# Kernel optimization log

Hardware: AMD Instinct MI355X
Metric: run time of the kernel (lower is better)

Reference implementation:

```python
import jax, jax.numpy as jnp
import numpy as np

B, V, F = 128, 256, 64      # batch, vertices, features-per-vertex
NS, NLR, K, NOUT = 4, 64, 40, 128
F_EFF = 2 * F               # cat_means doubles feature dim


def setup_inputs() -> dict:
    key = jax.random.key(0)
    k0, k1, k2 = jax.random.split(key, 3)
    x = jax.random.normal(k0, (B, V, F), dtype=jnp.float32)
    # f_slr: single Linear(F_EFF, NS+NLR) + ReLU (f_slr_depth=1)
    W_slr = jax.random.normal(k1, (F_EFF, NS + NLR), dtype=jnp.float32) / np.sqrt(F_EFF).astype(np.float32)
    b_slr = jnp.zeros((NS + NLR,), dtype=jnp.float32)
    # f_out: single Linear(F_EFF + 2*NLR, NOUT) + ReLU (f_out_depth=1, 2 agg methods)
    fin = F_EFF + 2 * NLR
    W_out = jax.random.normal(k2, (fin, NOUT), dtype=jnp.float32) / np.sqrt(fin).astype(np.float32)
    b_out = jnp.zeros((NOUT,), dtype=jnp.float32)
    return {"x": x, "W_slr": W_slr, "b_slr": b_slr, "W_out": W_out, "b_out": b_out}


def reference(x, W_slr, b_slr, W_out, b_out):
    # cat_means: append per-event feature means (broadcast over vertices)
    x = jnp.concatenate([x, jnp.broadcast_to(x.mean(axis=1, keepdims=True), x.shape)], axis=-1)  # (B,V,2F)
    slr = jax.nn.relu(x @ W_slr + b_slr)                    # (B,V,NS+NLR)
    s, lr = slr[..., :NS], slr[..., NS:]
    # pairwise squared distances in latent space (potential only needs d^2, so
    # we skip the sqrt: exp(-10*d^2) == exp(-10*d2), and kNN order is identical)
    diff = s[:, :, None, :] - s[:, None, :, :]              # (B,V,V,NS)
    d2 = jnp.sum(diff * diff, axis=-1)                      # (B,V,V)
    _, idx = jax.lax.top_k(-d2, K)                          # (B,V,K) k smallest (incl. self)
    d2k = jnp.take_along_axis(d2, idx, axis=2)              # (B,V,K)
    lr_nb = jax.vmap(lambda l, i: l[i])(lr, idx)            # (B,V,K,NLR)
    v = jnp.exp(-10.0 * d2k)                                # potential exp(-10 d^2)
    ft = lr_nb * v[..., None]                               # (B,V,K,NLR)
    fp = jnp.concatenate([x, ft.mean(axis=2), ft.max(axis=2)], axis=-1)  # (B,V,2F+2NLR)
    return jax.nn.relu(fp @ W_out + b_out)                  # (B,V,NOUT)
```

## Files before the change

### kernel.cpp

```cpp
#include <hip/hip_runtime.h>

constexpr int Bn = 128, Vn = 256, Fn = 64;
constexpr int NSLR = 68, NSn = 4, NLRn = 64;
constexpr int Kn = 40, NOUTn = 128;
constexpr int ROWS = Bn * Vn;

typedef __attribute__((ext_vector_type(8))) short short8;
typedef __attribute__((ext_vector_type(4))) float f32x4;

__device__ __forceinline__ int mbcnt64(unsigned long long m) {
  return __builtin_amdgcn_mbcnt_hi((unsigned)(m >> 32),
         __builtin_amdgcn_mbcnt_lo((unsigned)(m & 0xFFFFFFFFull), 0));
}

__device__ __forceinline__ unsigned short rneb(float v) {
  unsigned u = __float_as_uint(v);
  unsigned r = u + 0x7FFFu + ((u >> 16) & 1u);
  return (unsigned short)(r >> 16);
}
__device__ __forceinline__ float bf2f(unsigned short h) {
  return __uint_as_float(((unsigned)h) << 16);
}

__global__ __launch_bounds__(256) void kprep_w(const float* __restrict__ W_slr,
                                               const float* __restrict__ W_out,
                                               short* __restrict__ wt1h, short* __restrict__ wt1l,
                                               short* __restrict__ wt2h, short* __restrict__ wt2l) {
  int id = blockIdx.x * 256 + threadIdx.x;
  if (id < 16384) {
    int col = id >> 7, k = id & 127;
    float val = (col < NSLR) ? W_slr[k * NSLR + col] : 0.f;
    unsigned short h = rneb(val);
    unsigned short lo = rneb(val - bf2f(h));
    wt1h[id] = (short)h; wt1l[id] = (short)lo;
  } else {
    int id2 = id - 16384;
    int col = id2 >> 8, k = id2 & 255;
    float val = W_out[k * NOUTn + col];
    unsigned short h = rneb(val);
    unsigned short lo = rneb(val - bf2f(h));
    wt2h[id2] = (short)h; wt2l[id2] = (short)lo;
  }
}

__global__ __launch_bounds__(256) void kprep_x(const float* __restrict__ x,
                                               short* __restrict__ xhi, short* __restrict__ xlo,
                                               short* __restrict__ xmhi, short* __restrict__ xmlo) {
  const int b = blockIdx.x, t = threadIdx.x, f = t & 63, vg = t >> 6;
  const float* xb = x + (size_t)b * 16384;
  float sum = 0.f;
  for (int i = 0; i < 64; ++i) {
    int v = vg * 64 + i;
    float val = xb[v * 64 + f];
    sum += val;
    unsigned short h = rneb(val);
    unsigned short lo = rneb(val - bf2f(h));
    size_t o = (size_t)b * 16384 + v * 64 + f;
    xhi[o] = (short)h; xlo[o] = (short)lo;
  }
  __shared__ float ps[4][64];
  ps[vg][f] = sum;
  __syncthreads();
  if (t < 64) {
    float m = ((ps[0][f] + ps[1][f]) + (ps[2][f] + ps[3][f])) * (1.f / 256.f);
    unsigned short h = rneb(m);
    unsigned short lo = rneb(m - bf2f(h));
    xmhi[b * 64 + f] = (short)h; xmlo[b * 64 + f] = (short)lo;
  }
}

template <int NCH, bool IS_OUT>
__global__ __launch_bounds__(512) void kgemm_mfma(
    const short* __restrict__ xhi, const short* __restrict__ xlo,
    const short* __restrict__ xmhi, const short* __restrict__ xmlo,
    const short* __restrict__ fmh, const short* __restrict__ fml,
    const short* __restrict__ fxh, const short* __restrict__ fxl,
    const short* __restrict__ wth, const short* __restrict__ wtl,
    const float* __restrict__ bias,
    float* __restrict__ s_ws, float* __restrict__ lr_ws,
    float* __restrict__ outp) {
  constexpr int KTOT = NCH * 64;
  __shared__ __align__(16) short Ah[8192], Al[8192], Bh[8192], Bl[8192];
  const int t = threadIdx.x;
  const int l = t & 63;
  const int w = t >> 6;
  const int wr = w >> 2, wc = w & 3;
  const int rowBase = blockIdx.x * 128;
  const int b = rowBase >> 8;

  f32x4 acc[4][2];
#pragma unroll
  for (int mf = 0; mf < 4; ++mf)
#pragma unroll
    for (int nf = 0; nf < 2; ++nf) acc[mf][nf] = (f32x4)(0.f);

  const int lr8 = l >> 3;
  const int ul = (l & 7) ^ lr8;

#pragma unroll
  for (int kc = 0; kc < NCH; ++kc) {
    __syncthreads();
#pragma unroll
    for (int rep = 0; rep < 2; ++rep) {
      const int s = w + rep * 8;
      const int arow = s * 8 + lr8;
      const short *gah, *gal;
      if (kc == 0)      { size_t o = (size_t)(rowBase + arow) * 64 + ul * 8; gah = xhi + o;  gal = xlo + o; }
      else if (kc == 1) { size_t o = (size_t)b * 64 + ul * 8;                gah = xmhi + o; gal = xmlo + o; }
      else if (kc == 2) { size_t o = (size_t)(rowBase + arow) * 64 + ul * 8; gah = fmh + o;  gal = fml + o; }
      else              { size_t o = (size_t)(rowBase + arow) * 64 + ul * 8; gah = fxh + o;  gal = fxl + o; }
      __builtin_amdgcn_global_load_lds((const __attribute__((address_space(1))) void*)gah,
                                       (__attribute__((address_space(3))) void*)&Ah[s * 512], 16, 0, 0);
      __builtin_amdgcn_global_load_lds((const __attribute__((address_space(1))) void*)gal,
                                       (__attribute__((address_space(3))) void*)&Al[s * 512], 16, 0, 0);
      const short* gbh = wth + (size_t)arow * KTOT + kc * 64 + ul * 8;
      const short* gbl = wtl + (size_t)arow * KTOT + kc * 64 + ul * 8;
      __builtin_amdgcn_global_load_lds((const __attribute__((address_space(1))) void*)gbh,
                                       (__attribute__((address_space(3))) void*)&Bh[s * 512], 16, 0, 0);
      __builtin_amdgcn_global_load_lds((const __attribute__((address_space(1))) void*)gbl,
                                       (__attribute__((address_space(3))) void*)&Bl[s * 512], 16, 0, 0);
    }
    __syncthreads();
#pragma unroll
    for (int ks = 0; ks < 2; ++ks) {
      const int pu = (ks * 4 + (l >> 4)) ^ (l & 7);
      short8 ah[4], al[4], bh[2], bl[2];
#pragma unroll
      for (int mf = 0; mf < 4; ++mf) {
        int row = wr * 64 + mf * 16 + (l & 15);
        ah[mf] = *(const short8*)&Ah[row * 64 + pu * 8];
        al[mf] = *(const short8*)&Al[row * 64 + pu * 8];
      }
#pragma unroll
      for (int nf = 0; nf < 2; ++nf) {
        int col = wc * 32 + nf * 16 + (l & 15);
        bh[nf] = *(const short8*)&Bh[col * 64 + pu * 8];
        bl[nf] = *(const short8*)&Bl[col * 64 + pu * 8];
      }
#pragma unroll
      for (int mf = 0; mf < 4; ++mf)
#pragma unroll
        for (int nf = 0; nf < 2; ++nf) {
          acc[mf][nf] = __builtin_amdgcn_mfma_f32_16x16x32_bf16(ah[mf], bh[nf], acc[mf][nf], 0, 0, 0);
          acc[mf][nf] = __builtin_amdgcn_mfma_f32_16x16x32_bf16(ah[mf], bl[nf], acc[mf][nf], 0, 0, 0);
          acc[mf][nf] = __builtin_amdgcn_mfma_f32_16x16x32_bf16(al[mf], bh[nf], acc[mf][nf], 0, 0, 0);
        }
    }
  }
#pragma unroll
  for (int mf = 0; mf < 4; ++mf)
#pragma unroll
    for (int nf = 0; nf < 2; ++nf) {
      const int col = wc * 32 + nf * 16 + (l & 15);
      if (IS_OUT) {
        const float bia = bias[col];
#pragma unroll
        for (int r = 0; r < 4; ++r) {
          int row = rowBase + wr * 64 + mf * 16 + (l >> 4) * 4 + r;
          float vv = acc[mf][nf][r] + bia;
          outp[(size_t)row * NOUTn + col] = vv > 0.f ? vv : 0.f;
        }
      } else {
        if (col < NSLR) {
          const float bia = bias[col];
#pragma unroll
          for (int r = 0; r < 4; ++r) {
            int row = rowBase + wr * 64 + mf * 16 + (l >> 4) * 4 + r;
            float vv = acc[mf][nf][r] + bia;
            vv = vv > 0.f ? vv : 0.f;
            if (col < NSn) s_ws[b * 1024 + col * 256 + (row & 255)] = vv;
            else           lr_ws[(size_t)row * NLRn + (col - NSn)] = vv;
          }
        }
      }
    }
}

__global__ __launch_bounds__(256) void kselect(const float* __restrict__ s_ws,
                                               const float* __restrict__ lr_ws,
                                               short* __restrict__ fmh, short* __restrict__ fml,
                                               short* __restrict__ fxh, short* __restrict__ fxl) {
  __shared__ float sT[4][256];
  __shared__ unsigned int lst[4][Kn];
  const int id = blockIdx.x;
  const int xcd = id & 7;
  const int rrx = id >> 3;
  const int b = xcd + 8 * (rrx & 15);
  const int seg = rrx >> 4;
  const int t = threadIdx.x;
  const int lane = t & 63;
  const int w = t >> 6;

  {
    const float* sb = s_ws + b * 1024;
    sT[0][t] = sb[t]; sT[1][t] = sb[256 + t];
    sT[2][t] = sb[512 + t]; sT[3][t] = sb[768 + t];
  }
  __syncthreads();

  const float C = -14.4269504088896340736f;
  const float* lrbase = lr_ws + (size_t)b * (256 * NLRn) + lane;

  for (int it = 0; it < 4; ++it) {
    const int i = seg * 16 + w * 4 + it;
    const float si0 = sT[0][i], si1 = sT[1][i];
    const float si2 = sT[2][i], si3 = sT[3][i];
    unsigned int kb[4];
    float vv[4];
#pragma unroll
    for (int q = 0; q < 4; ++q) {
      int j = q * 64 + lane;
      float d0 = sT[0][j] - si0;
      float d1 = sT[1][j] - si1;
      float d2_ = sT[2][j] - si2;
      float d3 = sT[3][j] - si3;
      float dd = ((d0 * d0 + d1 * d1) + d2_ * d2_) + d3 * d3;
      kb[q] = __float_as_uint(dd);
      vv[q] = exp2f(C * dd);
    }
    unsigned int T = 0;
    for (int bit = 30; bit >= 0; --bit) {
      unsigned int cand = T | (1u << bit);
      int cnt = __popcll(__ballot(kb[0] < cand)) + __popcll(__ballot(kb[1] < cand)) +
                __popcll(__ballot(kb[2] < cand)) + __popcll(__ballot(kb[3] < cand));
      if (cnt < Kn) T = cand;
    }
    int nlt = __popcll(__ballot(kb[0] < T)) + __popcll(__ballot(kb[1] < T)) +
              __popcll(__ballot(kb[2] < T)) + __popcll(__ballot(kb[3] < T));
    int rem = Kn - nlt;
    int base = 0, ecum = 0;
#pragma unroll
    for (int q = 0; q < 4; ++q) {
      bool lt = kb[q] < T;
      bool eq = kb[q] == T;
      unsigned long long meq = __ballot(eq);
      int eqrank = ecum + mbcnt64(meq);
      bool sel = lt || (eq && (eqrank < rem));
      unsigned long long msel = __ballot(sel);
      int pos = base + mbcnt64(msel);
      if (sel)
        lst[w][pos] = (__float_as_uint(vv[q]) & 0xFFFFFF00u) | (unsigned)(q * 64 + lane);
      base += __popcll(msel);
      ecum += __popcll(meq);
    }
    float accm = 0.f, accx = 0.f;
#pragma unroll 8
    for (int tt = 0; tt < Kn; ++tt) {
      unsigned int p = lst[w][tt];
      int j = p & 0xFF;
      float v = __uint_as_float(p & 0xFFFFFF00u);
      float tv = v * lrbase[j * NLRn];
      accm += tv;
      accx = fmaxf(accx, tv);
    }
    accm *= (1.f / 40.f);
    size_t ro = ((size_t)(b * 256 + i)) * 64 + lane;
    unsigned short mh = rneb(accm);
    unsigned short ml = rneb(accm - bf2f(mh));
    unsigned short xh = rneb(accx);
    unsigned short xl = rneb(accx - bf2f(xh));
    fmh[ro] = (short)mh; fml[ro] = (short)ml;
    fxh[ro] = (short)xh; fxl[ro] = (short)xl;
  }
}

extern "C" void kernel_launch(void* const* d_in, const int* in_sizes, int n_in,
                              void* d_out, int out_size, void* d_ws, size_t ws_size,
                              hipStream_t stream) {
  const float* x = (const float*)d_in[0];
  const float* W_slr = (const float*)d_in[1];
  const float* b_slr = (const float*)d_in[2];
  const float* W_out = (const float*)d_in[3];
  const float* b_out = (const float*)d_in[4];
  float* out = (float*)d_out;

  char* p = (char*)d_ws;
  auto take = [&](size_t bytes) { char* c = p; p += (bytes + 255) & ~(size_t)255; return c; };
  short* xhi = (short*)take((size_t)ROWS * 64 * 2);
  short* xlo = (short*)take((size_t)ROWS * 64 * 2);
  short* xmhi = (short*)take(Bn * 64 * 2);
  short* xmlo = (short*)take(Bn * 64 * 2);
  short* wt1h = (short*)take(128 * 128 * 2);
  short* wt1l = (short*)take(128 * 128 * 2);
  short* wt2h = (short*)take(128 * 256 * 2);
  short* wt2l = (short*)take(128 * 256 * 2);
  float* s_ws = (float*)take(Bn * 1024 * 4);
  float* lr_ws = (float*)take((size_t)ROWS * 64 * 4);
  short* fmh = (short*)take((size_t)ROWS * 64 * 2);
  short* fml = (short*)take((size_t)ROWS * 64 * 2);
  short* fxh = (short*)take((size_t)ROWS * 64 * 2);
  short* fxl = (short*)take((size_t)ROWS * 64 * 2);

  kprep_w<<<192, 256, 0, stream>>>(W_slr, W_out, wt1h, wt1l, wt2h, wt2l);
  kprep_x<<<Bn, 256, 0, stream>>>(x, xhi, xlo, xmhi, xmlo);
  kgemm_mfma<2, false><<<ROWS / 128, 512, 0, stream>>>(
      xhi, xlo, xmhi, xmlo, nullptr, nullptr, nullptr, nullptr,
      wt1h, wt1l, b_slr, s_ws, lr_ws, nullptr);
  kselect<<<Bn * 16, 256, 0, stream>>>(s_ws, lr_ws, fmh, fml, fxh, fxl);
  kgemm_mfma<4, true><<<ROWS / 128, 512, 0, stream>>>(
      xhi, xlo, xmhi, xmlo, fmh, fml, fxh, fxl,
      wt2h, wt2l, b_out, nullptr, nullptr, out);
}
```

Baseline: 138.1 us.

## Fold mean features into per-batch bias and drop split-bf16 in output GEMM

```diff
diff --git a/kernel.cpp b/kernel.cpp
--- a/kernel.cpp
+++ b/kernel.cpp
@@ -4,6 +4,7 @@
 constexpr int NSLR = 68, NSn = 4, NLRn = 64;
 constexpr int Kn = 40, NOUTn = 128;
 constexpr int ROWS = Bn * Vn;
+constexpr int KB2 = 192;
 
 typedef __attribute__((ext_vector_type(8))) short short8;
 typedef __attribute__((ext_vector_type(4))) float f32x4;
@@ -12,7 +13,6 @@
   return __builtin_amdgcn_mbcnt_hi((unsigned)(m >> 32),
          __builtin_amdgcn_mbcnt_lo((unsigned)(m & 0xFFFFFFFFull), 0));
 }
-
 __device__ __forceinline__ unsigned short rneb(float v) {
   unsigned u = __float_as_uint(v);
   unsigned r = u + 0x7FFFu + ((u >> 16) & 1u);
@@ -21,165 +21,241 @@
 __device__ __forceinline__ float bf2f(unsigned short h) {
   return __uint_as_float(((unsigned)h) << 16);
 }
+#define GL_LDS(gp, lp) __builtin_amdgcn_global_load_lds( \
+    (const __attribute__((address_space(1))) void*)(gp), \
+    (__attribute__((address_space(3))) void*)(lp), 16, 0, 0)
 
 __global__ __launch_bounds__(256) void kprep_w(const float* __restrict__ W_slr,
                                                const float* __restrict__ W_out,
                                                short* __restrict__ wt1h, short* __restrict__ wt1l,
-                                               short* __restrict__ wt2h, short* __restrict__ wt2l) {
-  int id = blockIdx.x * 256 + threadIdx.x;
-  if (id < 16384) {
-    int col = id >> 7, k = id & 127;
-    float val = (col < NSLR) ? W_slr[k * NSLR + col] : 0.f;
+                                               short* __restrict__ wt2) {
+  const int col = blockIdx.x;
+  const int t = threadIdx.x;
+  if (t < 64) {
+    float val = (col < NSLR) ? W_slr[t * NSLR + col] : 0.f;
     unsigned short h = rneb(val);
-    unsigned short lo = rneb(val - bf2f(h));
-    wt1h[id] = (short)h; wt1l[id] = (short)lo;
+    wt1h[col * 64 + t] = (short)h;
+    wt1l[col * 64 + t] = (short)rneb(val - bf2f(h));
   } else {
-    int id2 = id - 16384;
-    int col = id2 >> 8, k = id2 & 255;
-    float val = W_out[k * NOUTn + col];
-    unsigned short h = rneb(val);
-    unsigned short lo = rneb(val - bf2f(h));
-    wt2h[id2] = (short)h; wt2l[id2] = (short)lo;
+    int k = t - 64;
+    int row = (k < 64) ? k : 64 + k;
+    wt2[col * KB2 + k] = (short)rneb(W_out[row * NOUTn + col]);
   }
 }
 
 __global__ __launch_bounds__(256) void kprep_x(const float* __restrict__ x,
                                                short* __restrict__ xhi, short* __restrict__ xlo,
-                                               short* __restrict__ xmhi, short* __restrict__ xmlo) {
-  const int b = blockIdx.x, t = threadIdx.x, f = t & 63, vg = t >> 6;
-  const float* xb = x + (size_t)b * 16384;
-  float sum = 0.f;
-  for (int i = 0; i < 64; ++i) {
-    int v = vg * 64 + i;
-    float val = xb[v * 64 + f];
-    sum += val;
-    unsigned short h = rneb(val);
-    unsigned short lo = rneb(val - bf2f(h));
-    size_t o = (size_t)b * 16384 + v * 64 + f;
-    xhi[o] = (short)h; xlo[o] = (short)lo;
-  }
-  __shared__ float ps[4][64];
-  ps[vg][f] = sum;
+                                               float* __restrict__ xmean) {
+  const int b = blockIdx.x, t = threadIdx.x;
+  const int f4 = t & 15, vg = t >> 4;
+  const float4* xb = (const float4*)(x + (size_t)b * 16384);
+  float4 sum = make_float4(0.f, 0.f, 0.f, 0.f);
+  for (int i = 0; i < 16; ++i) {
+    int v = vg * 16 + i;
+    float4 val = xb[v * 16 + f4];
+    sum.x += val.x; sum.y += val.y; sum.z += val.z; sum.w += val.w;
+    unsigned short h0 = rneb(val.x), h1 = rneb(val.y), h2 = rneb(val.z), h3 = rneb(val.w);
+    short4 hi = {(short)h0, (short)h1, (short)h2, (short)h3};
+    short4 lo = {(short)rneb(val.x - bf2f(h0)), (short)rneb(val.y - bf2f(h1)),
+                 (short)rneb(val.z - bf2f(h2)), (short)rneb(val.w - bf2f(h3))};
+    size_t o = (size_t)b * 4096 + v * 16 + f4;
+    ((short4*)xhi)[o] = hi;
+    ((short4*)xlo)[o] = lo;
+  }
+  __shared__ float4 ps[16][16];
+  ps[vg][f4] = sum;
   __syncthreads();
-  if (t < 64) {
-    float m = ((ps[0][f] + ps[1][f]) + (ps[2][f] + ps[3][f])) * (1.f / 256.f);
-    unsigned short h = rneb(m);
-    unsigned short lo = rneb(m - bf2f(h));
-    xmhi[b * 64 + f] = (short)h; xmlo[b * 64 + f] = (short)lo;
-  }
-}
-
-template <int NCH, bool IS_OUT>
-__global__ __launch_bounds__(512) void kgemm_mfma(
+  if (t < 16) {
+    float4 m = ps[0][t];
+    for (int g = 1; g < 16; ++g) {
+      float4 v = ps[g][t];
+      m.x += v.x; m.y += v.y; m.z += v.z; m.w += v.w;
+    }
+    m.x *= (1.f / 256.f); m.y *= (1.f / 256.f); m.z *= (1.f / 256.f); m.w *= (1.f / 256.f);
+    ((float4*)xmean)[b * 16 + t] = m;
+  }
+}
+
+__global__ __launch_bounds__(256) void kbias(const float* __restrict__ xmean,
+                                             const float* __restrict__ W_slr,
+                                             const float* __restrict__ b_slr,
+                                             const float* __restrict__ W_out,
+                                             const float* __restrict__ b_out,
+                                             float* __restrict__ bias1,
+                                             float* __restrict__ bias2) {
+  const int b = blockIdx.x, t = threadIdx.x;
+  __shared__ float xm[64];
+  if (t < 64) xm[t] = xmean[b * 64 + t];
+  __syncthreads();
+  if (t < 128) {
+    float acc = b_out[t];
+    for (int f = 0; f < 64; ++f) acc = fmaf(xm[f], W_out[(64 + f) * NOUTn + t], acc);
+    bias2[b * 128 + t] = acc;
+  } else {
+    int c = t - 128;
+    float acc = 0.f;
+    if (c < NSLR) {
+      acc = b_slr[c];
+      for (int f = 0; f < 64; ++f) acc = fmaf(xm[f], W_slr[(64 + f) * NSLR + c], acc);
+    }
+    bias1[b * 128 + c] = acc;
+  }
+}
+
+__global__ __launch_bounds__(256) void kgemm1(
     const short* __restrict__ xhi, const short* __restrict__ xlo,
-    const short* __restrict__ xmhi, const short* __restrict__ xmlo,
-    const short* __restrict__ fmh, const short* __restrict__ fml,
-    const short* __restrict__ fxh, const short* __restrict__ fxl,
-    const short* __restrict__ wth, const short* __restrict__ wtl,
-    const float* __restrict__ bias,
-    float* __restrict__ s_ws, float* __restrict__ lr_ws,
-    float* __restrict__ outp) {
-  constexpr int KTOT = NCH * 64;
-  __shared__ __align__(16) short Ah[8192], Al[8192], Bh[8192], Bl[8192];
-  const int t = threadIdx.x;
-  const int l = t & 63;
-  const int w = t >> 6;
-  const int wr = w >> 2, wc = w & 3;
-  const int rowBase = blockIdx.x * 128;
+    const short* __restrict__ wt1h, const short* __restrict__ wt1l,
+    const float* __restrict__ bias1,
+    float* __restrict__ s_ws, float* __restrict__ lr_ws) {
+  __shared__ __align__(16) short Ah[4096], Al[4096], Bh[8192], Bl[8192];
+  const int t = threadIdx.x, l = t & 63, w = t >> 6;
+  const int wr = w >> 1, wc = w & 1;
+  const int rowBase = blockIdx.x * 64;
   const int b = rowBase >> 8;
-
-  f32x4 acc[4][2];
-#pragma unroll
-  for (int mf = 0; mf < 4; ++mf)
-#pragma unroll
-    for (int nf = 0; nf < 2; ++nf) acc[mf][nf] = (f32x4)(0.f);
-
-  const int lr8 = l >> 3;
-  const int ul = (l & 7) ^ lr8;
-
-#pragma unroll
-  for (int kc = 0; kc < NCH; ++kc) {
+  const int lr8 = l >> 3, ul = (l & 7) ^ lr8;
+
+#pragma unroll
+  for (int rep = 0; rep < 2; ++rep) {
+    const int seg = w + rep * 4;
+    size_t o = (size_t)(rowBase + seg * 8 + lr8) * 64 + ul * 8;
+    GL_LDS(xhi + o, &Ah[seg * 512]);
+    GL_LDS(xlo + o, &Al[seg * 512]);
+  }
+#pragma unroll
+  for (int rep = 0; rep < 4; ++rep) {
+    const int seg = w + rep * 4;
+    size_t o = (size_t)(seg * 8 + lr8) * 64 + ul * 8;
+    GL_LDS(wt1h + o, &Bh[seg * 512]);
+    GL_LDS(wt1l + o, &Bl[seg * 512]);
+  }
+  __syncthreads();
+
+  f32x4 acc[2][4];
+#pragma unroll
+  for (int mf = 0; mf < 2; ++mf)
+#pragma unroll
+    for (int nf = 0; nf < 4; ++nf) acc[mf][nf] = (f32x4)(0.f);
+
+#pragma unroll
+  for (int ks = 0; ks < 2; ++ks) {
+    short8 ah[2], al[2], bh[4], bl[4];
+#pragma unroll
+    for (int mf = 0; mf < 2; ++mf) {
+      int row = wr * 32 + mf * 16 + (l & 15);
+      int pu = (ks * 4 + (l >> 4)) ^ (row & 7);
+      ah[mf] = *(const short8*)&Ah[row * 64 + pu * 8];
+      al[mf] = *(const short8*)&Al[row * 64 + pu * 8];
+    }
+#pragma unroll
+    for (int nf = 0; nf < 4; ++nf) {
+      int col = wc * 64 + nf * 16 + (l & 15);
+      int pu = (ks * 4 + (l >> 4)) ^ (col & 7);
+      bh[nf] = *(const short8*)&Bh[col * 64 + pu * 8];
+      bl[nf] = *(const short8*)&Bl[col * 64 + pu * 8];
+    }
+#pragma unroll
+    for (int mf = 0; mf < 2; ++mf)
+#pragma unroll
+      for (int nf = 0; nf < 4; ++nf) {
+        acc[mf][nf] = __builtin_amdgcn_mfma_f32_16x16x32_bf16(ah[mf], bh[nf], acc[mf][nf], 0, 0, 0);
+        acc[mf][nf] = __builtin_amdgcn_mfma_f32_16x16x32_bf16(ah[mf], bl[nf], acc[mf][nf], 0, 0, 0);
+        acc[mf][nf] = __builtin_amdgcn_mfma_f32_16x16x32_bf16(al[mf], bh[nf], acc[mf][nf], 0, 0, 0);
+      }
+  }
+#pragma unroll
+  for (int mf = 0; mf < 2; ++mf)
+#pragma unroll
+    for (int nf = 0; nf < 4; ++nf) {
+      const int col = wc * 64 + nf * 16 + (l & 15);
+      if (col < NSLR) {
+        const float bia = bias1[b * 128 + col];
+#pragma unroll
+        for (int r = 0; r < 4; ++r) {
+          int row = rowBase + wr * 32 + mf * 16 + (l >> 4) * 4 + r;
+          float vv = acc[mf][nf][r] + bia;
+          vv = vv > 0.f ? vv : 0.f;
+          if (col < NSn) s_ws[b * 1024 + col * 256 + (row & 255)] = vv;
+          else           lr_ws[(size_t)row * NLRn + (col - NSn)] = vv;
+        }
+      }
+    }
+}
+
+__global__ __launch_bounds__(256) void kgemm2(
+    const short* __restrict__ xhi, const short* __restrict__ fm,
+    const short* __restrict__ fx, const short* __restrict__ wt2,
+    const float* __restrict__ bias2, float* __restrict__ outp) {
+  __shared__ __align__(16) short As[4096], Bs[8192];
+  const int t = threadIdx.x, l = t & 63, w = t >> 6;
+  const int wr = w >> 1, wc = w & 1;
+  const int rowBase = blockIdx.x * 64;
+  const int b = rowBase >> 8;
+  const int lr8 = l >> 3, ul = (l & 7) ^ lr8;
+
+  f32x4 acc[2][4];
+#pragma unroll
+  for (int mf = 0; mf < 2; ++mf)
+#pragma unroll
+    for (int nf = 0; nf < 4; ++nf) acc[mf][nf] = (f32x4)(0.f);
+
+#pragma unroll
+  for (int kc = 0; kc < 3; ++kc) {
     __syncthreads();
+    const short* asrc = (kc == 0) ? xhi : (kc == 1) ? fm : fx;
 #pragma unroll
     for (int rep = 0; rep < 2; ++rep) {
-      const int s = w + rep * 8;
-      const int arow = s * 8 + lr8;
-      const short *gah, *gal;
-      if (kc == 0)      { size_t o = (size_t)(rowBase + arow) * 64 + ul * 8; gah = xhi + o;  gal = xlo + o; }
-      else if (kc == 1) { size_t o = (size_t)b * 64 + ul * 8;                gah = xmhi + o; gal = xmlo + o; }
-      else if (kc == 2) { size_t o = (size_t)(rowBase + arow) * 64 + ul * 8; gah = fmh + o;  gal = fml + o; }
-      else              { size_t o = (size_t)(rowBase + arow) * 64 + ul * 8; gah = fxh + o;  gal = fxl + o; }
-      __builtin_amdgcn_global_load_lds((const __attribute__((address_space(1))) void*)gah,
-                                       (__attribute__((address_space(3))) void*)&Ah[s * 512], 16, 0, 0);
-      __builtin_amdgcn_global_load_lds((const __attribute__((address_space(1))) void*)gal,
-                                       (__attribute__((address_space(3))) void*)&Al[s * 512], 16, 0, 0);
-      const short* gbh = wth + (size_t)arow * KTOT + kc * 64 + ul * 8;
-      const short* gbl = wtl + (size_t)arow * KTOT + kc * 64 + ul * 8;
-      __builtin_amdgcn_global_load_lds((const __attribute__((address_space(1))) void*)gbh,
-                                       (__attribute__((address_space(3))) void*)&Bh[s * 512], 16, 0, 0);
-      __builtin_amdgcn_global_load_lds((const __attribute__((address_space(1))) void*)gbl,
-                                       (__attribute__((address_space(3))) void*)&Bl[s * 512], 16, 0, 0);
+      const int seg = w + rep * 4;
+      size_t o = (size_t)(rowBase + seg * 8 + lr8) * 64 + ul * 8;
+      GL_LDS(asrc + o, &As[seg * 512]);
+    }
+#pragma unroll
+    for (int rep = 0; rep < 4; ++rep) {
+      const int seg = w + rep * 4;
+      size_t o = (size_t)(seg * 8 + lr8) * KB2 + kc * 64 + ul * 8;
+      GL_LDS(wt2 + o, &Bs[seg * 512]);
     }
     __syncthreads();
 #pragma unroll
     for (int ks = 0; ks < 2; ++ks) {
-      const int pu = (ks * 4 + (l >> 4)) ^ (l & 7);
-      short8 ah[4], al[4], bh[2], bl[2];
-#pragma unroll
-      for (int mf = 0; mf < 4; ++mf) {
-        int row = wr * 64 + mf * 16 + (l & 15);
-        ah[mf] = *(const short8*)&Ah[row * 64 + pu * 8];
-        al[mf] = *(const short8*)&Al[row * 64 + pu * 8];
-      }
-#pragma unroll
-      for (int nf = 0; nf < 2; ++nf) {
-        int col = wc * 32 + nf * 16 + (l & 15);
-        bh[nf] = *(const short8*)&Bh[col * 64 + pu * 8];
-        bl[nf] = *(const short8*)&Bl[col * 64 + pu * 8];
-      }
-#pragma unroll
-      for (int mf = 0; mf < 4; ++mf)
-#pragma unroll
-        for (int nf = 0; nf < 2; ++nf) {
-          acc[mf][nf] = __builtin_amdgcn_mfma_f32_16x16x32_bf16(ah[mf], bh[nf], acc[mf][nf], 0, 0, 0);
-          acc[mf][nf] = __builtin_amdgcn_mfma_f32_16x16x32_bf16(ah[mf], bl[nf], acc[mf][nf], 0, 0, 0);
-          acc[mf][nf] = __builtin_amdgcn_mfma_f32_16x16x32_bf16(al[mf], bh[nf], acc[mf][nf], 0, 0, 0);
-        }
-    }
-  }
-#pragma unroll
-  for (int mf = 0; mf < 4; ++mf)
-#pragma unroll
-    for (int nf = 0; nf < 2; ++nf) {
-      const int col = wc * 32 + nf * 16 + (l & 15);
-      if (IS_OUT) {
-        const float bia = bias[col];
-#pragma unroll
-        for (int r = 0; r < 4; ++r) {
-          int row = rowBase + wr * 64 + mf * 16 + (l >> 4) * 4 + r;
-          float vv = acc[mf][nf][r] + bia;
-          outp[(size_t)row * NOUTn + col] = vv > 0.f ? vv : 0.f;
-        }
-      } else {
-        if (col < NSLR) {
-          const float bia = bias[col];
-#pragma unroll
-          for (int r = 0; r < 4; ++r) {
-            int row = rowBase + wr * 64 + mf * 16 + (l >> 4) * 4 + r;
-            float vv = acc[mf][nf][r] + bia;
-            vv = vv > 0.f ? vv : 0.f;
-            if (col < NSn) s_ws[b * 1024 + col * 256 + (row & 255)] = vv;
-            else           lr_ws[(size_t)row * NLRn + (col - NSn)] = vv;
-          }
-        }
+      short8 a[2], bb[4];
+#pragma unroll
+      for (int mf = 0; mf < 2; ++mf) {
+        int row = wr * 32 + mf * 16 + (l & 15);
+        int pu = (ks * 4 + (l >> 4)) ^ (row & 7);
+        a[mf] = *(const short8*)&As[row * 64 + pu * 8];
+      }
+#pragma unroll
+      for (int nf = 0; nf < 4; ++nf) {
+        int col = wc * 64 + nf * 16 + (l & 15);
+        int pu = (ks * 4 + (l >> 4)) ^ (col & 7);
+        bb[nf] = *(const short8*)&Bs[col * 64 + pu * 8];
+      }
+#pragma unroll
+      for (int mf = 0; mf < 2; ++mf)
+#pragma unroll
+        for (int nf = 0; nf < 4; ++nf)
+          acc[mf][nf] = __builtin_amdgcn_mfma_f32_16x16x32_bf16(a[mf], bb[nf], acc[mf][nf], 0, 0, 0);
+    }
+  }
+#pragma unroll
+  for (int mf = 0; mf < 2; ++mf)
+#pragma unroll
+    for (int nf = 0; nf < 4; ++nf) {
+      const int col = wc * 64 + nf * 16 + (l & 15);
+      const float bia = bias2[b * 128 + col];
+#pragma unroll
+      for (int r = 0; r < 4; ++r) {
+        int row = rowBase + wr * 32 + mf * 16 + (l >> 4) * 4 + r;
+        float vv = acc[mf][nf][r] + bia;
+        outp[(size_t)row * NOUTn + col] = vv > 0.f ? vv : 0.f;
       }
     }
 }
 
 __global__ __launch_bounds__(256) void kselect(const float* __restrict__ s_ws,
                                                const float* __restrict__ lr_ws,
-                                               short* __restrict__ fmh, short* __restrict__ fml,
-                                               short* __restrict__ fxh, short* __restrict__ fxl) {
+                                               short* __restrict__ fm,
+                                               short* __restrict__ fx) {
   __shared__ float sT[4][256];
   __shared__ unsigned int lst[4][Kn];
   const int id = blockIdx.x;
@@ -187,9 +263,7 @@
   const int rrx = id >> 3;
   const int b = xcd + 8 * (rrx & 15);
   const int seg = rrx >> 4;
-  const int t = threadIdx.x;
-  const int lane = t & 63;
-  const int w = t >> 6;
+  const int t = threadIdx.x, lane = t & 63, w = t >> 6;
 
   {
     const float* sb = s_ws + b * 1024;
@@ -253,14 +327,9 @@
       accm += tv;
       accx = fmaxf(accx, tv);
     }
-    accm *= (1.f / 40.f);
     size_t ro = ((size_t)(b * 256 + i)) * 64 + lane;
-    unsigned short mh = rneb(accm);
-    unsigned short ml = rneb(accm - bf2f(mh));
-    unsigned short xh = rneb(accx);
-    unsigned short xl = rneb(accx - bf2f(xh));
-    fmh[ro] = (short)mh; fml[ro] = (short)ml;
-    fxh[ro] = (short)xh; fxl[ro] = (short)xl;
+    fm[ro] = (short)rneb(accm * (1.f / 40.f));
+    fx[ro] = (short)rneb(accx);
   }
 }
 
@@ -278,26 +347,21 @@
   auto take = [&](size_t bytes) { char* c = p; p += (bytes + 255) & ~(size_t)255; return c; };
   short* xhi = (short*)take((size_t)ROWS * 64 * 2);
   short* xlo = (short*)take((size_t)ROWS * 64 * 2);
-  short* xmhi = (short*)take(Bn * 64 * 2);
-  short* xmlo = (short*)take(Bn * 64 * 2);
-  short* wt1h = (short*)take(128 * 128 * 2);
-  short* wt1l = (short*)take(128 * 128 * 2);
-  short* wt2h = (short*)take(128 * 256 * 2);
-  short* wt2l = (short*)take(128 * 256 * 2);
+  float* xmean = (float*)take(Bn * 64 * 4);
+  short* wt1h = (short*)take(128 * 64 * 2);
+  short* wt1l = (short*)take(128 * 64 * 2);
+  short* wt2 = (short*)take(128 * KB2 * 2);
+  float* bias1 = (float*)take(Bn * 128 * 4);
+  float* bias2 = (float*)take(Bn * 128 * 4);
   float* s_ws = (float*)take(Bn * 1024 * 4);
   float* lr_ws = (float*)take((size_t)ROWS * 64 * 4);
-  short* fmh = (short*)take((size_t)ROWS * 64 * 2);
-  short* fml = (short*)take((size_t)ROWS * 64 * 2);
-  short* fxh = (short*)take((size_t)ROWS * 64 * 2);
-  short* fxl = (short*)take((size_t)ROWS * 64 * 2);
-
-  kprep_w<<<192, 256, 0, stream>>>(W_slr, W_out, wt1h, wt1l, wt2h, wt2l);
-  kprep_x<<<Bn, 256, 0, stream>>>(x, xhi, xlo, xmhi, xmlo);
-  kgemm_mfma<2, false><<<ROWS / 128, 512, 0, stream>>>(
-      xhi, xlo, xmhi, xmlo, nullptr, nullptr, nullptr, nullptr,
-      wt1h, wt1l, b_slr, s_ws, lr_ws, nullptr);
-  kselect<<<Bn * 16, 256, 0, stream>>>(s_ws, lr_ws, fmh, fml, fxh, fxl);
-  kgemm_mfma<4, true><<<ROWS / 128, 512, 0, stream>>>(
-      xhi, xlo, xmhi, xmlo, fmh, fml, fxh, fxl,
-      wt2h, wt2l, b_out, nullptr, nullptr, out);
-}
+  short* fm = (short*)take((size_t)ROWS * 64 * 2);
+  short* fx = (short*)take((size_t)ROWS * 64 * 2);
+
+  kprep_w<<<128, 256, 0, stream>>>(W_slr, W_out, wt1h, wt1l, wt2);
+  kprep_x<<<Bn, 256, 0, stream>>>(x, xhi, xlo, xmean);
+  kbias<<<Bn, 256, 0, stream>>>(xmean, W_slr, b_slr, W_out, b_out, bias1, bias2);
+  kgemm1<<<ROWS / 64, 256, 0, stream>>>(xhi, xlo, wt1h, wt1l, bias1, s_ws, lr_ws);
+  kselect<<<Bn * 16, 256, 0, stream>>>(s_ws, lr_ws, fm, fx);
+  kgemm2<<<ROWS / 64, 256, 0, stream>>>(xhi, fm, fx, wt2, bias2, out);
+}
```

Result: faster. 133.6 us (-3.3%).
